# Kernel optimization log

Hardware: AMD Instinct MI355X
Metric: run time of the kernel (lower is better)

## Reference

```python
import jax, jax.numpy as jnp
import numpy as np

EPS = 1e-8  # torch F.cosine_similarity default eps


def setup_inputs() -> dict:
    key = jax.random.key(0)
    k1, k2 = jax.random.split(key)
    B, D, C = 8192, 1024, 1000
    x = jax.random.normal(k1, (B, D), dtype=jnp.float32)
    W = jax.random.normal(k2, (D, C), dtype=jnp.float32) * 0.02
    b = jnp.zeros((C,), dtype=jnp.float32)
    return {"x": x, "W": W, "b": b}


def reference(x, W, b):
    B = x.shape[0]
    # classifier logits -> softmax probs
    logits = x @ W + b                              # [B, C]
    logp = jax.nn.log_softmax(logits, axis=1)       # [B, C]
    pred = jnp.exp(logp)
    # per-row sum of p * log p (negative entropy), matches pred*log(pred) loop
    loss = jnp.sum(pred * logp, axis=-1)            # [B]
    # per-row mean cosine similarity against all rows (incl. self)
    norms = jnp.maximum(jnp.linalg.norm(x, axis=1, keepdims=True), EPS)
    xn = x / norms                                  # [B, D]
    sim = xn @ xn.T                                 # [B, B]
    weight = jnp.sum(sim, axis=1) / B               # [B]
    return loss * weight
```

## Files before the change

kernel.cpp:

```cpp
#include <hip/hip_runtime.h>
#include <hip/hip_bf16.h>
#include <cstdint>
#include <cstddef>

typedef __attribute__((ext_vector_type(8))) short bf16x8;
typedef __attribute__((ext_vector_type(4))) float f32x4;

__device__ __forceinline__ unsigned short f2bf(float f) {
  union { float f; unsigned u; } v; v.f = f;
  unsigned r = v.u + 0x7FFFu + ((v.u >> 16) & 1u);
  return (unsigned short)(r >> 16);
}

__device__ __forceinline__ float bf2f(unsigned short h) {
  union { float f; unsigned u; } c; c.u = ((unsigned)h) << 16;
  return c.f;
}

__device__ __forceinline__ void gload_lds16(const void* g, void* l) {
  __builtin_amdgcn_global_load_lds(
      (const __attribute__((address_space(1))) unsigned int*)g,
      (__attribute__((address_space(3))) unsigned int*)l, 16, 0, 0);
}

__global__ __launch_bounds__(1024) void k01_prep(const float* __restrict__ W,
                                                 unsigned short* __restrict__ Wt,
                                                 const float* __restrict__ x,
                                                 unsigned short* __restrict__ xbf,
                                                 float* __restrict__ rnorm,
                                                 float* __restrict__ s) {
  __shared__ __align__(16) char sm[82176];
  int tid = threadIdx.x;
  int b = blockIdx.x;
  int lane = tid & 63;
  int wid = tid >> 6;

  int k0 = (b & 15) * 64;
  int c0 = (b >> 4) * 64;
  int tx = tid & 63;
  int ty = tid >> 6;
  float wreg[4];
#pragma unroll
  for (int i = 0; i < 4; ++i) {
    int c = c0 + tx;
    wreg[i] = (c < 1000) ? W[(size_t)(k0 + i * 16 + ty) * 1000 + c] : 0.f;
  }

  {
    float (*sblk)[1024] = (float(*)[1024])sm;
    int row0 = b * 32 + wid * 2;
    const float4* xr0 = (const float4*)(x + (size_t)row0 * 1024);
    const float4* xr1 = (const float4*)(x + (size_t)(row0 + 1) * 1024);
    float4 v[2][4];
#pragma unroll
    for (int j = 0; j < 4; ++j) v[0][j] = xr0[lane + j * 64];
#pragma unroll
    for (int j = 0; j < 4; ++j) v[1][j] = xr1[lane + j * 64];
    float ss0 = 0.f, ss1 = 0.f;
#pragma unroll
    for (int j = 0; j < 4; ++j) {
      ss0 += v[0][j].x * v[0][j].x + v[0][j].y * v[0][j].y +
             v[0][j].z * v[0][j].z + v[0][j].w * v[0][j].w;
      ss1 += v[1][j].x * v[1][j].x + v[1][j].y * v[1][j].y +
             v[1][j].z * v[1][j].z + v[1][j].w * v[1][j].w;
    }
#pragma unroll
    for (int m = 1; m < 64; m <<= 1) {
      ss0 += __shfl_xor(ss0, m);
      ss1 += __shfl_xor(ss1, m);
    }
    float rn0 = 1.f / fmaxf(sqrtf(ss0), 1e-8f);
    float rn1 = 1.f / fmaxf(sqrtf(ss1), 1e-8f);
    if (lane == 0) {
      rnorm[row0] = rn0;
      rnorm[row0 + 1] = rn1;
    }
    float4 sacc[4];
#pragma unroll
    for (int j = 0; j < 4; ++j) {
      ushort4 h0, h1;
      h0.x = f2bf(v[0][j].x); h0.y = f2bf(v[0][j].y);
      h0.z = f2bf(v[0][j].z); h0.w = f2bf(v[0][j].w);
      h1.x = f2bf(v[1][j].x); h1.y = f2bf(v[1][j].y);
      h1.z = f2bf(v[1][j].z); h1.w = f2bf(v[1][j].w);
      ((ushort4*)(xbf + (size_t)row0 * 1024))[lane + j * 64] = h0;
      ((ushort4*)(xbf + (size_t)(row0 + 1) * 1024))[lane + j * 64] = h1;
      sacc[j].x = v[0][j].x * rn0 + v[1][j].x * rn1;
      sacc[j].y = v[0][j].y * rn0 + v[1][j].y * rn1;
      sacc[j].z = v[0][j].z * rn0 + v[1][j].z * rn1;
      sacc[j].w = v[0][j].w * rn0 + v[1][j].w * rn1;
    }
#pragma unroll
    for (int j = 0; j < 4; ++j) ((float4*)sblk[wid])[j * 64 + lane] = sacc[j];
    __syncthreads();
    float t = 0.f;
#pragma unroll
    for (int w = 0; w < 16; ++w) t += sblk[w][tid];
    atomicAdd(&s[tid], t);
  }

  {
    float (*tile)[65] = (float(*)[65])(sm + 65536);
#pragma unroll
    for (int i = 0; i < 4; ++i) tile[i * 16 + ty][tx] = wreg[i];
    __syncthreads();
#pragma unroll
    for (int i = 0; i < 4; ++i) {
      int ct = i * 16 + ty;
      Wt[(size_t)(c0 + ct) * 1024 + (k0 + tx)] = f2bf(tile[tx][ct]);
    }
  }
}

#define LDSBUF 49152

__global__ __launch_bounds__(512) void k3_gemm(const unsigned short* __restrict__ xbf,
                                               const unsigned short* __restrict__ wt,
                                               const float* __restrict__ bias,
                                               float* __restrict__ pm,
                                               float* __restrict__ pz,
                                               float* __restrict__ ps) {
  __shared__ __align__(16) char lds[147456];

  int tid = threadIdx.x;
  int lane = tid & 63;
  int wid = tid >> 6;
  int wc = wid & 1;
  int wr = wid >> 1;
  int cb = blockIdx.x >> 5;
  int rb = blockIdx.x & 31;
  int C0 = cb * 128;
  int R0 = rb * 256;

  float bv[4][4];
#pragma unroll
  for (int mf = 0; mf < 4; ++mf)
#pragma unroll
    for (int q = 0; q < 4; ++q) {
      int cls_g = C0 + wc * 64 + mf * 16 + (lane >> 4) * 4 + q;
      bv[mf][q] = (cls_g < 1000) ? bias[cls_g] : -1e30f;
    }
  f32x4 acc[4][4];
#pragma unroll
  for (int mf = 0; mf < 4; ++mf)
#pragma unroll
    for (int nf = 0; nf < 4; ++nf)
#pragma unroll
      for (int q = 0; q < 4; ++q) acc[mf][nf][q] = bv[mf][q];

  const char* gA = (const char*)(wt + (size_t)C0 * 1024);
  const char* gB = (const char*)(xbf + (size_t)R0 * 1024);
  int grow = lane >> 3;
  int gswz = ((lane & 7) ^ grow) << 4;

#define STA(kt, b, r)                                                          \
  gload_lds16(gA + (size_t)((r) * 64 + wid * 8 + grow) * 2048 + (kt) * 128 +   \
                  gswz,                                                        \
              lds + (b) * LDSBUF + (r) * 8192 + wid * 1024)
#define STB(kt, b, r)                                                          \
  gload_lds16(gB + (size_t)((r) * 64 + wid * 8 + grow) * 2048 + (kt) * 128 +   \
                  gswz,                                                        \
              lds + (b) * LDSBUF + 16384 + (r) * 8192 + wid * 1024)

  STA(0, 0, 0); STA(0, 0, 1); STB(0, 0, 0); STB(0, 0, 1); STB(0, 0, 2); STB(0, 0, 3);
  STA(1, 1, 0); STA(1, 1, 1); STB(1, 1, 0); STB(1, 1, 1); STB(1, 1, 2); STB(1, 1, 3);

  int rsw = (lane & 7) << 4;
  int kcol = (lane >> 4) * 16;

  auto ktile = [&](const char* A, const char* B, int nt, int nb, bool pf) {
    bf16x8 a[4][2];
#pragma unroll
    for (int mf = 0; mf < 4; ++mf)
#pragma unroll
      for (int ks = 0; ks < 2; ++ks)
        a[mf][ks] = *(const bf16x8*)(A + (wc * 64 + mf * 16 + (lane & 15)) * 128 +
                                     ((ks * 64 + kcol) ^ rsw));
    {
      bf16x8 b0[2];
#pragma unroll
      for (int ks = 0; ks < 2; ++ks)
        b0[ks] = *(const bf16x8*)(B + (wr * 64 + 0 * 16 + (lane & 15)) * 128 +
                                  ((ks * 64 + kcol) ^ rsw));
      if (pf) { STA(nt, nb, 0); STA(nt, nb, 1); }
      __builtin_amdgcn_s_barrier();
      __builtin_amdgcn_s_setprio(1);
#pragma unroll
      for (int ks = 0; ks < 2; ++ks)
#pragma unroll
        for (int mf = 0; mf < 4; ++mf)
          acc[mf][0] = __builtin_amdgcn_mfma_f32_16x16x32_bf16(a[mf][ks], b0[ks],
                                                               acc[mf][0], 0, 0, 0);
      __builtin_amdgcn_s_setprio(0);
      __builtin_amdgcn_s_barrier();
    }
    {
      bf16x8 b1[2];
#pragma unroll
      for (int ks = 0; ks < 2; ++ks)
        b1[ks] = *(const bf16x8*)(B + (wr * 64 + 1 * 16 + (lane & 15)) * 128 +
                                  ((ks * 64 + kcol) ^ rsw));
      if (pf) { STB(nt, nb, 0); STB(nt, nb, 1); }
      __builtin_amdgcn_s_barrier();
      __builtin_amdgcn_s_setprio(1);
#pragma unroll
      for (int ks = 0; ks < 2; ++ks)
#pragma unroll
        for (int mf = 0; mf < 4; ++mf)
          acc[mf][1] = __builtin_amdgcn_mfma_f32_16x16x32_bf16(a[mf][ks], b1[ks],
                                                               acc[mf][1], 0, 0, 0);
      __builtin_amdgcn_s_setprio(0);
      __builtin_amdgcn_s_barrier();
    }
    {
      bf16x8 b2[2];
#pragma unroll
      for (int ks = 0; ks < 2; ++ks)
        b2[ks] = *(const bf16x8*)(B + (wr * 64 + 2 * 16 + (lane & 15)) * 128 +
                                  ((ks * 64 + kcol) ^ rsw));
      if (pf) { STB(nt, nb, 2); STB(nt, nb, 3); }
      __builtin_amdgcn_s_barrier();
      __builtin_amdgcn_s_setprio(1);
#pragma unroll
      for (int ks = 0; ks < 2; ++ks)
#pragma unroll
        for (int mf = 0; mf < 4; ++mf)
          acc[mf][2] = __builtin_amdgcn_mfma_f32_16x16x32_bf16(a[mf][ks], b2[ks],
                                                               acc[mf][2], 0, 0, 0);
      __builtin_amdgcn_s_setprio(0);
      __builtin_amdgcn_s_barrier();
    }
    {
      bf16x8 b3[2];
#pragma unroll
      for (int ks = 0; ks < 2; ++ks)
        b3[ks] = *(const bf16x8*)(B + (wr * 64 + 3 * 16 + (lane & 15)) * 128 +
                                  ((ks * 64 + kcol) ^ rsw));
      __builtin_amdgcn_s_barrier();
      __builtin_amdgcn_s_setprio(1);
#pragma unroll
      for (int ks = 0; ks < 2; ++ks)
#pragma unroll
        for (int mf = 0; mf < 4; ++mf)
          acc[mf][3] = __builtin_amdgcn_mfma_f32_16x16x32_bf16(a[mf][ks], b3[ks],
                                                               acc[mf][3], 0, 0, 0);
      __builtin_amdgcn_s_setprio(0);
    }
  };

  for (int t = 0; t < 15; ++t) {
    asm volatile("s_waitcnt vmcnt(6)" ::: "memory");
    __builtin_amdgcn_s_barrier();
    asm volatile("" ::: "memory");
    const char* A = lds + (t % 3) * LDSBUF;
    ktile(A, A + 16384, t + 2, (t + 2) % 3, t < 14);
  }
  asm volatile("s_waitcnt vmcnt(0)" ::: "memory");
  __builtin_amdgcn_s_barrier();
  asm volatile("" ::: "memory");
  {
    const char* A = lds + (15 % 3) * LDSBUF;
    ktile(A, A + 16384, 0, 0, false);
  }

  __syncthreads();
  float* mm = (float*)lds;
  float* zz = mm + 512;
  float* sv = zz + 512;
#pragma unroll
  for (int nf = 0; nf < 4; ++nf) {
    float m1 = -1e30f;
#pragma unroll
    for (int mf = 0; mf < 4; ++mf)
#pragma unroll
      for (int q = 0; q < 4; ++q) m1 = fmaxf(m1, acc[mf][nf][q]);
    m1 = fmaxf(m1, __shfl_xor(m1, 16));
    m1 = fmaxf(m1, __shfl_xor(m1, 32));
    float z1 = 0.f, s1 = 0.f;
#pragma unroll
    for (int mf = 0; mf < 4; ++mf)
#pragma unroll
      for (int q = 0; q < 4; ++q) {
        float tt = acc[mf][nf][q] - m1;
        float e = expf(tt);
        z1 += e;
        s1 += e * tt;
      }
    z1 += __shfl_xor(z1, 16); z1 += __shfl_xor(z1, 32);
    s1 += __shfl_xor(s1, 16); s1 += __shfl_xor(s1, 32);
    if (lane < 16) {
      int r = wr * 64 + nf * 16 + lane;
      mm[wc * 256 + r] = m1;
      zz[wc * 256 + r] = z1;
      sv[wc * 256 + r] = s1;
    }
  }
  __syncthreads();
  if (tid < 256) {
    float m0 = mm[tid], mA = mm[256 + tid];
    float z0 = zz[tid], zA = zz[256 + tid];
    float s0 = sv[tid], sA = sv[256 + tid];
    float M = fmaxf(m0, mA);
    float e0 = expf(m0 - M), e1 = expf(mA - M);
    float Z = z0 * e0 + zA * e1;
    float S = e0 * (s0 + (m0 - M) * z0) + e1 * (sA + (mA - M) * zA);
    size_t o = (size_t)cb * 8192 + R0 + tid;
    pm[o] = M;
    pz[o] = Z;
    ps[o] = S;
  }
}

__global__ __launch_bounds__(256) void k4_final(const unsigned short* __restrict__ xbf,
                                                const float* __restrict__ s,
                                                const float* __restrict__ rnorm,
                                                const float* __restrict__ pm,
                                                const float* __restrict__ pz,
                                                const float* __restrict__ ps,
                                                float* __restrict__ out) {
  int tid = threadIdx.x;
  int wid = tid >> 6, lane = tid & 63;
  int row = blockIdx.x * 4 + wid;
  const bf16x8* xr = (const bf16x8*)(xbf + (size_t)row * 1024);
  const float4* s4 = (const float4*)s;
  float dot = 0.f;
#pragma unroll
  for (int j = 0; j < 2; ++j) {
    bf16x8 v = xr[lane + j * 64];
    float4 sa = s4[(lane + j * 64) * 2];
    float4 sb = s4[(lane + j * 64) * 2 + 1];
    dot += bf2f((unsigned short)v[0]) * sa.x + bf2f((unsigned short)v[1]) * sa.y +
           bf2f((unsigned short)v[2]) * sa.z + bf2f((unsigned short)v[3]) * sa.w +
           bf2f((unsigned short)v[4]) * sb.x + bf2f((unsigned short)v[5]) * sb.y +
           bf2f((unsigned short)v[6]) * sb.z + bf2f((unsigned short)v[7]) * sb.w;
  }
#pragma unroll
  for (int m = 1; m < 64; m <<= 1) dot += __shfl_xor(dot, m);
  if (lane == 0) {
    float mv[8], zv[8], svv[8];
    float M = -1e30f;
#pragma unroll
    for (int c = 0; c < 8; ++c) {
      mv[c] = pm[(size_t)c * 8192 + row];
      zv[c] = pz[(size_t)c * 8192 + row];
      svv[c] = ps[(size_t)c * 8192 + row];
      M = fmaxf(M, mv[c]);
    }
    float Z = 0.f, S = 0.f;
#pragma unroll
    for (int c = 0; c < 8; ++c) {
      float e = expf(mv[c] - M);
      Z += zv[c] * e;
      S += e * (svv[c] + (mv[c] - M) * zv[c]);
    }
    float loss = S / Z - logf(Z);
    out[row] = loss * dot * rnorm[row] * (1.f / 8192.f);
  }
}

extern "C" void kernel_launch(void* const* d_in, const int* in_sizes, int n_in,
                              void* d_out, int out_size, void* d_ws, size_t ws_size,
                              hipStream_t stream) {
  (void)in_sizes; (void)n_in; (void)out_size; (void)ws_size;
  const float* x = (const float*)d_in[0];
  const float* W = (const float*)d_in[1];
  const float* b = (const float*)d_in[2];
  float* out = (float*)d_out;
  char* ws = (char*)d_ws;

  unsigned short* Wt = (unsigned short*)(ws + 0);
  unsigned short* xbf = (unsigned short*)(ws + 2097152);
  float* rnorm = (float*)(ws + 18874368);
  float* s = (float*)(ws + 18907136);
  float* pm = (float*)(ws + 18915328);
  float* pz = (float*)(ws + 18915328 + 262144);
  float* ps = (float*)(ws + 18915328 + 524288);

  hipMemsetAsync(s, 0, 4096, stream);
  k01_prep<<<256, 1024, 0, stream>>>(W, Wt, x, xbf, rnorm, s);
  k3_gemm<<<256, 512, 0, stream>>>(xbf, Wt, b, pm, pz, ps);
  k4_final<<<2048, 256, 0, stream>>>(xbf, s, rnorm, pm, pz, ps, out);
}
```

Before: 52.22 us.

## Fold similarity-sum dot into GEMM as extra class; drop atomics and GEMM barriers

The per-row dot with the column sum of normalized rows is computed inside the classifier GEMM. A new reduction kernel writes the bf16 column-sum vector into unused padded row 1000 of the transposed weight. That logit is extracted into a separate buffer and masked out of the softmax. The atomic accumulation and its memset are replaced by per-block partial sums reduced in that new kernel, and the final kernel becomes a thin elementwise combine. Inside the GEMM k-tile, the per-fragment s_barriers are removed and the prefetches are issued earlier. This cuts sync overhead but risks LDS races and adds one small launch.

```diff
diff --git a/kernel.cpp b/kernel.cpp
--- a/kernel.cpp
+++ b/kernel.cpp
@@ -28,7 +28,7 @@
                                                  const float* __restrict__ x,
                                                  unsigned short* __restrict__ xbf,
                                                  float* __restrict__ rnorm,
-                                                 float* __restrict__ s) {
+                                                 float* __restrict__ sp) {
   __shared__ __align__(16) char sm[82176];
   int tid = threadIdx.x;
   int b = blockIdx.x;
@@ -93,10 +93,10 @@
 #pragma unroll
     for (int j = 0; j < 4; ++j) ((float4*)sblk[wid])[j * 64 + lane] = sacc[j];
     __syncthreads();
-    float t = 0.f;
-#pragma unroll
-    for (int w = 0; w < 16; ++w) t += sblk[w][tid];
-    atomicAdd(&s[tid], t);
+    float acc = 0.f;
+#pragma unroll
+    for (int w = 0; w < 16; ++w) acc += sblk[w][tid];
+    sp[(size_t)b * 1024 + tid] = acc;
   }
 
   {
@@ -109,6 +109,26 @@
       int ct = i * 16 + ty;
       Wt[(size_t)(c0 + ct) * 1024 + (k0 + tx)] = f2bf(tile[tx][ct]);
     }
+  }
+}
+
+__global__ __launch_bounds__(256) void k2_sred(const float* __restrict__ sp,
+                                               float* __restrict__ s,
+                                               unsigned short* __restrict__ Wt) {
+  __shared__ float red[4][64];
+  int t = threadIdx.x;
+  int dd = t & 63;
+  int g = t >> 6;
+  int d = blockIdx.x * 64 + dd;
+  float acc = 0.f;
+#pragma unroll 8
+  for (int b = g * 64; b < g * 64 + 64; ++b) acc += sp[(size_t)b * 1024 + d];
+  red[g][dd] = acc;
+  __syncthreads();
+  if (g == 0) {
+    float sv = red[0][dd] + red[1][dd] + red[2][dd] + red[3][dd];
+    s[d] = sv;
+    Wt[(size_t)1000 * 1024 + d] = f2bf(sv);
   }
 }
 
@@ -119,7 +139,8 @@
                                                const float* __restrict__ bias,
                                                float* __restrict__ pm,
                                                float* __restrict__ pz,
-                                               float* __restrict__ ps) {
+                                               float* __restrict__ ps,
+                                               float* __restrict__ pd) {
   __shared__ __align__(16) char lds[147456];
 
   int tid = threadIdx.x;
@@ -138,7 +159,7 @@
 #pragma unroll
     for (int q = 0; q < 4; ++q) {
       int cls_g = C0 + wc * 64 + mf * 16 + (lane >> 4) * 4 + q;
-      bv[mf][q] = (cls_g < 1000) ? bias[cls_g] : -1e30f;
+      bv[mf][q] = (cls_g < 1000) ? bias[cls_g] : ((cls_g == 1000) ? 0.f : -1e30f);
     }
   f32x4 acc[4][4];
 #pragma unroll
@@ -169,6 +190,7 @@
   int kcol = (lane >> 4) * 16;
 
   auto ktile = [&](const char* A, const char* B, int nt, int nb, bool pf) {
+    if (pf) { STA(nt, nb, 0); STA(nt, nb, 1); }
     bf16x8 a[4][2];
 #pragma unroll
     for (int mf = 0; mf < 4; ++mf)
@@ -182,8 +204,6 @@
       for (int ks = 0; ks < 2; ++ks)
         b0[ks] = *(const bf16x8*)(B + (wr * 64 + 0 * 16 + (lane & 15)) * 128 +
                                   ((ks * 64 + kcol) ^ rsw));
-      if (pf) { STA(nt, nb, 0); STA(nt, nb, 1); }
-      __builtin_amdgcn_s_barrier();
       __builtin_amdgcn_s_setprio(1);
 #pragma unroll
       for (int ks = 0; ks < 2; ++ks)
@@ -192,16 +212,14 @@
           acc[mf][0] = __builtin_amdgcn_mfma_f32_16x16x32_bf16(a[mf][ks], b0[ks],
                                                                acc[mf][0], 0, 0, 0);
       __builtin_amdgcn_s_setprio(0);
-      __builtin_amdgcn_s_barrier();
-    }
+    }
+    if (pf) { STB(nt, nb, 0); STB(nt, nb, 1); }
     {
       bf16x8 b1[2];
 #pragma unroll
       for (int ks = 0; ks < 2; ++ks)
         b1[ks] = *(const bf16x8*)(B + (wr * 64 + 1 * 16 + (lane & 15)) * 128 +
                                   ((ks * 64 + kcol) ^ rsw));
-      if (pf) { STB(nt, nb, 0); STB(nt, nb, 1); }
-      __builtin_amdgcn_s_barrier();
       __builtin_amdgcn_s_setprio(1);
 #pragma unroll
       for (int ks = 0; ks < 2; ++ks)
@@ -210,16 +228,14 @@
           acc[mf][1] = __builtin_amdgcn_mfma_f32_16x16x32_bf16(a[mf][ks], b1[ks],
                                                                acc[mf][1], 0, 0, 0);
       __builtin_amdgcn_s_setprio(0);
-      __builtin_amdgcn_s_barrier();
-    }
+    }
+    if (pf) { STB(nt, nb, 2); STB(nt, nb, 3); }
     {
       bf16x8 b2[2];
 #pragma unroll
       for (int ks = 0; ks < 2; ++ks)
         b2[ks] = *(const bf16x8*)(B + (wr * 64 + 2 * 16 + (lane & 15)) * 128 +
                                   ((ks * 64 + kcol) ^ rsw));
-      if (pf) { STB(nt, nb, 2); STB(nt, nb, 3); }
-      __builtin_amdgcn_s_barrier();
       __builtin_amdgcn_s_setprio(1);
 #pragma unroll
       for (int ks = 0; ks < 2; ++ks)
@@ -228,7 +244,6 @@
           acc[mf][2] = __builtin_amdgcn_mfma_f32_16x16x32_bf16(a[mf][ks], b2[ks],
                                                                acc[mf][2], 0, 0, 0);
       __builtin_amdgcn_s_setprio(0);
-      __builtin_amdgcn_s_barrier();
     }
     {
       bf16x8 b3[2];
@@ -236,7 +251,6 @@
       for (int ks = 0; ks < 2; ++ks)
         b3[ks] = *(const bf16x8*)(B + (wr * 64 + 3 * 16 + (lane & 15)) * 128 +
                                   ((ks * 64 + kcol) ^ rsw));
-      __builtin_amdgcn_s_barrier();
       __builtin_amdgcn_s_setprio(1);
 #pragma unroll
       for (int ks = 0; ks < 2; ++ks)
@@ -261,6 +275,15 @@
   {
     const char* A = lds + (15 % 3) * LDSBUF;
     ktile(A, A + 16384, 0, 0, false);
+  }
+
+  if (cb == 7 && wc == 1 && ((lane >> 4) == 2)) {
+#pragma unroll
+    for (int nf = 0; nf < 4; ++nf) {
+      int r = wr * 64 + nf * 16 + (lane & 15);
+      pd[(size_t)rb * 256 + r] = acc[2][nf][0];
+      acc[2][nf][0] = -1e30f;
+    }
   }
 
   __syncthreads();
@@ -311,51 +334,31 @@
   }
 }
 
-__global__ __launch_bounds__(256) void k4_final(const unsigned short* __restrict__ xbf,
-                                                const float* __restrict__ s,
-                                                const float* __restrict__ rnorm,
+__global__ __launch_bounds__(256) void k4_final(const float* __restrict__ rnorm,
                                                 const float* __restrict__ pm,
                                                 const float* __restrict__ pz,
                                                 const float* __restrict__ ps,
+                                                const float* __restrict__ pd,
                                                 float* __restrict__ out) {
-  int tid = threadIdx.x;
-  int wid = tid >> 6, lane = tid & 63;
-  int row = blockIdx.x * 4 + wid;
-  const bf16x8* xr = (const bf16x8*)(xbf + (size_t)row * 1024);
-  const float4* s4 = (const float4*)s;
-  float dot = 0.f;
-#pragma unroll
-  for (int j = 0; j < 2; ++j) {
-    bf16x8 v = xr[lane + j * 64];
-    float4 sa = s4[(lane + j * 64) * 2];
-    float4 sb = s4[(lane + j * 64) * 2 + 1];
-    dot += bf2f((unsigned short)v[0]) * sa.x + bf2f((unsigned short)v[1]) * sa.y +
-           bf2f((unsigned short)v[2]) * sa.z + bf2f((unsigned short)v[3]) * sa.w +
-           bf2f((unsigned short)v[4]) * sb.x + bf2f((unsigned short)v[5]) * sb.y +
-           bf2f((unsigned short)v[6]) * sb.z + bf2f((unsigned short)v[7]) * sb.w;
-  }
-#pragma unroll
-  for (int m = 1; m < 64; m <<= 1) dot += __shfl_xor(dot, m);
-  if (lane == 0) {
-    float mv[8], zv[8], svv[8];
-    float M = -1e30f;
-#pragma unroll
-    for (int c = 0; c < 8; ++c) {
-      mv[c] = pm[(size_t)c * 8192 + row];
-      zv[c] = pz[(size_t)c * 8192 + row];
-      svv[c] = ps[(size_t)c * 8192 + row];
-      M = fmaxf(M, mv[c]);
-    }
-    float Z = 0.f, S = 0.f;
-#pragma unroll
-    for (int c = 0; c < 8; ++c) {
-      float e = expf(mv[c] - M);
-      Z += zv[c] * e;
-      S += e * (svv[c] + (mv[c] - M) * zv[c]);
-    }
-    float loss = S / Z - logf(Z);
-    out[row] = loss * dot * rnorm[row] * (1.f / 8192.f);
-  }
+  int row = blockIdx.x * 256 + threadIdx.x;
+  float mv[8], zv[8], svv[8];
+  float M = -1e30f;
+#pragma unroll
+  for (int c = 0; c < 8; ++c) {
+    mv[c] = pm[(size_t)c * 8192 + row];
+    zv[c] = pz[(size_t)c * 8192 + row];
+    svv[c] = ps[(size_t)c * 8192 + row];
+    M = fmaxf(M, mv[c]);
+  }
+  float Z = 0.f, S = 0.f;
+#pragma unroll
+  for (int c = 0; c < 8; ++c) {
+    float e = expf(mv[c] - M);
+    Z += zv[c] * e;
+    S += e * (svv[c] + (mv[c] - M) * zv[c]);
+  }
+  float loss = S / Z - logf(Z);
+  out[row] = loss * pd[row] * rnorm[row] * (1.f / 8192.f);
 }
 
 extern "C" void kernel_launch(void* const* d_in, const int* in_sizes, int n_in,
@@ -372,12 +375,14 @@
   unsigned short* xbf = (unsigned short*)(ws + 2097152);
   float* rnorm = (float*)(ws + 18874368);
   float* s = (float*)(ws + 18907136);
+  float* sp = (float*)(ws + 18915328);
   float* pm = (float*)(ws + 18915328);
   float* pz = (float*)(ws + 18915328 + 262144);
   float* ps = (float*)(ws + 18915328 + 524288);
-
-  hipMemsetAsync(s, 0, 4096, stream);
-  k01_prep<<<256, 1024, 0, stream>>>(W, Wt, x, xbf, rnorm, s);
-  k3_gemm<<<256, 512, 0, stream>>>(xbf, Wt, b, pm, pz, ps);
-  k4_final<<<2048, 256, 0, stream>>>(xbf, s, rnorm, pm, pz, ps, out);
-}
+  float* pd = (float*)(ws + 18915328 + 786432);
+
+  k01_prep<<<256, 1024, 0, stream>>>(W, Wt, x, xbf, rnorm, sp);
+  k2_sred<<<16, 256, 0, stream>>>(sp, s, Wt);
+  k3_gemm<<<256, 512, 0, stream>>>(xbf, Wt, b, pm, pz, ps, pd);
+  k4_final<<<32, 256, 0, stream>>>(rnorm, pm, pz, ps, pd, out);
+}
```

Result: faster. 46.34 us (median of 2 runs) (-11.3%).
